# Performance work log

Hardware: AMD Instinct MI355X
Metric: run time of the kernel (lower is better)

## Reference

```python
import jax, jax.numpy as jnp
import numpy as np

N_HEAD = 16

def setup_inputs() -> dict:
    key = jax.random.key(0)
    ks = jax.random.split(key, 7)
    B, T, C = 2, 2048, 1024
    return {
        "query": jax.random.normal(ks[0], (B, T, C), jnp.float32),
        "key": jax.random.normal(ks[1], (B, T, C), jnp.float32),
        "value": jax.random.normal(ks[2], (B, T, C), jnp.float32),
        "Wq": jax.random.normal(ks[3], (C, C), jnp.float32) * (1.0 / np.sqrt(C)),
        "Wk": jax.random.normal(ks[4], (C, C), jnp.float32) * (1.0 / np.sqrt(C)),
        "Wv": jax.random.normal(ks[5], (C, C), jnp.float32) * (1.0 / np.sqrt(C)),
        "Wo": jax.random.normal(ks[6], (C, C), jnp.float32) * (1.0 / np.sqrt(C)),
    }

def reference(query, key, value, Wq, Wk, Wv, Wo):
    B, T, C = query.shape
    H = N_HEAD
    D = C // H
    # QKV projections (torch Linear: x @ W.T, no bias)
    q = (query @ Wq.T).reshape(B, T, H, D).transpose(0, 2, 1, 3)  # [B,H,T,D]
    k = (key   @ Wk.T).reshape(B, T, H, D).transpose(0, 2, 1, 3)
    v = (value @ Wv.T).reshape(B, T, H, D).transpose(0, 2, 1, 3)
    scale = 1.0 / np.sqrt(D).astype(np.float32)
    att = jnp.einsum("bhqd,bhkd->bhqk", q, k) * scale  # [B,H,T,T]
    att = jax.nn.softmax(att, axis=-1)
    y = jnp.einsum("bhqk,bhkd->bhqd", att, v)  # [B,H,T,D]
    y = y.transpose(0, 2, 1, 3).reshape(B, T, C)
    return y @ Wo.T
```

## Files before the change

kernel.cpp:

```cpp
#include <hip/hip_runtime.h>
#include <hip/hip_bf16.h>
#include <cstdint>

typedef __attribute__((ext_vector_type(8))) short bf16x8;
typedef __attribute__((ext_vector_type(4))) float f32x4;
typedef __attribute__((ext_vector_type(16))) float f32x16;
typedef __attribute__((ext_vector_type(4))) unsigned short us4;

#define MFMA16(a, b, c) __builtin_amdgcn_mfma_f32_16x16x32_bf16((a), (b), (c), 0, 0, 0)
#define MFMA32(a, b, c) __builtin_amdgcn_mfma_f32_32x32x16_bf16((a), (b), (c), 0, 0, 0)
#define GLB_PTR(p) ((const __attribute__((address_space(1))) void*)(p))
#define LDS_PTR(p) ((__attribute__((address_space(3))) void*)(p))
#define WAITV(n) asm volatile("s_waitcnt vmcnt(" #n ")" ::: "memory")

__device__ __forceinline__ unsigned short f2bf(float f) {
    union { float f; unsigned u; } v; v.f = f;
    unsigned r = v.u + 0x7fffu + ((v.u >> 16) & 1u);
    return (unsigned short)(r >> 16);
}

__device__ __forceinline__ unsigned cvtpk(float lo, float hi) {
    unsigned r;
    asm("v_cvt_pk_bf16_f32 %0, %1, %2" : "=v"(r) : "v"(lo), "v"(hi));
    return r;
}

struct CastArgs {
    const float* src[7];
    unsigned short* dst[7];
    int n4[7];
};

__global__ __launch_bounds__(256) void cast_f32_bf16(CastArgs a) {
    const int id = blockIdx.y;
    const float4* s = (const float4*)a.src[id];
    us4* d = (us4*)a.dst[id];
    const int n4 = a.n4[id];
    for (int i = blockIdx.x * blockDim.x + threadIdx.x; i < n4;
         i += gridDim.x * blockDim.x) {
        float4 v = s[i];
        us4 o;
        o.x = f2bf(v.x); o.y = f2bf(v.y); o.z = f2bf(v.z); o.w = f2bf(v.w);
        d[i] = o;
    }
}

struct GemmGroup {
    const unsigned short* A[3];
    const unsigned short* B[3];
    unsigned short* C[3];
};

__global__ __launch_bounds__(256, 2)
void gemm_qkv(GemmGroup gg, int M, int N, int K) {
    __shared__ __align__(16) unsigned short As[3][128 * 32];
    __shared__ __align__(16) unsigned short Bs[3][128 * 32];
    const int z = blockIdx.z;
    const unsigned short* __restrict__ A = gg.A[z];
    const unsigned short* __restrict__ B = gg.B[z];
    unsigned short* __restrict__ C = gg.C[z];
    const int t = threadIdx.x;
    const int lane = t & 63, wave = t >> 6;
    const int row0 = blockIdx.x * 128, col0 = blockIdx.y * 128;
    const int wr = (wave >> 1) * 64, wc = (wave & 1) * 64;
    const int r = lane & 15, g = lane >> 4;
    const int srow = t >> 2;
    const int scol = (t & 3) * 8;

#define GSTAGE(sl, k0)                                                         \
    {                                                                          \
        _Pragma("unroll")                                                      \
        for (int i = 0; i < 2; ++i) {                                          \
            const int rr = i * 64 + srow;                                      \
            __builtin_amdgcn_global_load_lds(                                  \
                GLB_PTR(A + (size_t)(row0 + rr) * K + (k0) + scol),            \
                LDS_PTR(&As[sl][rr * 32 + scol]), 16, 0, 0);                   \
            __builtin_amdgcn_global_load_lds(                                  \
                GLB_PTR(B + (size_t)(col0 + rr) * K + (k0) + scol),            \
                LDS_PTR(&Bs[sl][rr * 32 + scol]), 16, 0, 0);                   \
        }                                                                      \
    }

    f32x4 acc[4][4] = {};
    GSTAGE(0, 0);
    GSTAGE(1, 32);

    for (int it = 0; it < 32; ++it) {
        if (it < 31) WAITV(4); else WAITV(0);
        __builtin_amdgcn_s_barrier();
        __builtin_amdgcn_sched_barrier(0);
        if (it + 2 < 32) GSTAGE((it + 2) % 3, (it + 2) * 32);
        const int sl = it % 3;
        bf16x8 a[4], b[4];
#pragma unroll
        for (int m = 0; m < 4; ++m)
            a[m] = *(const bf16x8*)(&As[sl][(wr + m * 16 + r) * 32 + g * 8]);
#pragma unroll
        for (int n = 0; n < 4; ++n)
            b[n] = *(const bf16x8*)(&Bs[sl][(wc + n * 16 + r) * 32 + g * 8]);
        __builtin_amdgcn_s_setprio(1);
#pragma unroll
        for (int m = 0; m < 4; ++m)
#pragma unroll
            for (int n = 0; n < 4; ++n)
                acc[m][n] = MFMA16(a[m], b[n], acc[m][n]);
        __builtin_amdgcn_s_setprio(0);
    }
#undef GSTAGE

    const float sc = (z == 0) ? 0.18033688011112042f : 1.0f;
#pragma unroll
    for (int m = 0; m < 4; ++m) {
#pragma unroll
        for (int n = 0; n < 4; ++n) {
#pragma unroll
            for (int i = 0; i < 4; ++i) {
                const int row = row0 + wr + m * 16 + g * 4 + i;
                const int col = col0 + wc + n * 16 + r;
                const int b_ = row >> 11, tt = row & 2047;
                const int h = col >> 6, d = col & 63;
                const int bh = b_ * 16 + h;
                size_t idx;
                if (z == 2) {
                    const int l = (d & 31) + 32 * ((tt >> 3) & 1);
                    idx = ((((size_t)(bh * 32 + (tt >> 6))) * 2 + (d >> 5)) * 4 +
                           ((tt >> 4) & 3)) * 512 + l * 8 + (tt & 7);
                } else {
                    const int l = (tt & 31) + 32 * ((d >> 3) & 1);
                    idx = (((size_t)(bh * 64 + (tt >> 5))) * 4 + (d >> 4)) * 512 +
                          l * 8 + (d & 7);
                }
                C[idx] = f2bf(acc[m][n][i] * sc);
            }
        }
    }
}

__global__ __launch_bounds__(256, 2)
void gemm_wo(const unsigned short* __restrict__ A,
             const unsigned short* __restrict__ B,
             float* __restrict__ C, int M, int N, int K) {
    __shared__ __align__(16) unsigned short As[3][64 * 32];
    __shared__ __align__(16) unsigned short Bs[3][128 * 32];
    const int t = threadIdx.x;
    const int lane = t & 63, wave = t >> 6;
    const int row0 = blockIdx.x * 64, col0 = blockIdx.y * 128;
    const int wc = wave * 32;
    const int r = lane & 15, g = lane >> 4;
    const int srow = t >> 2;
    const int scol = (t & 3) * 8;

#define WSTAGE(sl, k0)                                                         \
    {                                                                          \
        __builtin_amdgcn_global_load_lds(                                      \
            GLB_PTR(A + (size_t)(row0 + srow) * K + (k0) + scol),              \
            LDS_PTR(&As[sl][srow * 32 + scol]), 16, 0, 0);                     \
        _Pragma("unroll")                                                      \
        for (int i = 0; i < 2; ++i) {                                          \
            const int rr = i * 64 + srow;                                      \
            __builtin_amdgcn_global_load_lds(                                  \
                GLB_PTR(B + (size_t)(col0 + rr) * K + (k0) + scol),            \
                LDS_PTR(&Bs[sl][rr * 32 + scol]), 16, 0, 0);                   \
        }                                                                      \
    }

    f32x4 acc[4][2] = {};
    WSTAGE(0, 0);
    WSTAGE(1, 32);

    for (int it = 0; it < 32; ++it) {
        if (it < 31) WAITV(3); else WAITV(0);
        __builtin_amdgcn_s_barrier();
        __builtin_amdgcn_sched_barrier(0);
        if (it + 2 < 32) WSTAGE((it + 2) % 3, (it + 2) * 32);
        const int sl = it % 3;
        bf16x8 a[4], b[2];
#pragma unroll
        for (int m = 0; m < 4; ++m)
            a[m] = *(const bf16x8*)(&As[sl][(m * 16 + r) * 32 + g * 8]);
#pragma unroll
        for (int n = 0; n < 2; ++n)
            b[n] = *(const bf16x8*)(&Bs[sl][(wc + n * 16 + r) * 32 + g * 8]);
        __builtin_amdgcn_s_setprio(1);
#pragma unroll
        for (int m = 0; m < 4; ++m)
#pragma unroll
            for (int n = 0; n < 2; ++n)
                acc[m][n] = MFMA16(a[m], b[n], acc[m][n]);
        __builtin_amdgcn_s_setprio(0);
    }
#undef WSTAGE

#pragma unroll
    for (int m = 0; m < 4; ++m)
#pragma unroll
        for (int n = 0; n < 2; ++n)
#pragma unroll
            for (int i = 0; i < 4; ++i) {
                const int row = row0 + m * 16 + g * 4 + i;
                const int col = col0 + wc + n * 16 + r;
                C[(size_t)row * N + col] = acc[m][n][i];
            }
}

__global__ __launch_bounds__(256, 2)
void attn_fwd(const unsigned short* __restrict__ Qpk,
              const unsigned short* __restrict__ Kpk,
              const unsigned short* __restrict__ Vpk,
              unsigned short* __restrict__ Y) {
    __shared__ __align__(16) unsigned short kv_lds[4][16][512];
    const int t = threadIdx.x, lane = t & 63, w = t >> 6;
    const int q31 = lane & 31, hi = lane >> 5;

    const int flat = blockIdx.x;
    const int swz = (flat & 7) * 64 + (flat >> 3);
    const int qt = swz & 15, bh = swz >> 4;
    const int qb0 = qt * 128;

    const unsigned short* Qb = Qpk + ((size_t)(bh * 64 + qt * 4 + w)) * 2048;
    const unsigned short* Kb = Kpk + (size_t)bh * 131072;
    const unsigned short* Vb = Vpk + (size_t)bh * 131072;

    bf16x8 qf[4];
#pragma unroll
    for (int s = 0; s < 4; ++s)
        qf[s] = *(const bf16x8*)(Qb + s * 512 + lane * 8);
    WAITV(0);

    f32x16 o0 = {}, o1 = {};
    float l_ = 0.f;

#define STAGE(sl, kv0)                                                         \
    {                                                                          \
        _Pragma("unroll")                                                      \
        for (int i = 0; i < 4; ++i) {                                          \
            const int f = w * 4 + i;                                           \
            const unsigned short* src =                                        \
                (f < 8 ? Kb : Vb) + (kv0) * 64 + (f & 7) * 512 + lane * 8;     \
            __builtin_amdgcn_global_load_lds(                                  \
                GLB_PTR(src), LDS_PTR(&kv_lds[sl][f][lane * 8]), 16, 0, 0);    \
        }                                                                      \
    }

    STAGE(0, 0);
    STAGE(1, 64);
    STAGE(2, 128);

    WAITV(8);
    __builtin_amdgcn_s_barrier();
    __builtin_amdgcn_sched_barrier(0);
    f32x16 sA0, sA1;
    {
        bf16x8 kf[8];
#pragma unroll
        for (int i = 0; i < 8; ++i)
            kf[i] = *(const bf16x8*)(&kv_lds[0][i][lane * 8]);
#pragma unroll
        for (int r = 0; r < 16; ++r) { sA0[r] = -12.f; sA1[r] = -12.f; }
        __builtin_amdgcn_s_setprio(1);
#pragma unroll
        for (int s = 0; s < 4; ++s) sA0 = MFMA32(kf[s], qf[s], sA0);
#pragma unroll
        for (int s = 0; s < 4; ++s) sA1 = MFMA32(kf[4 + s], qf[s], sA1);
        __builtin_amdgcn_s_setprio(0);
    }

    for (int it = 0; it < 32; ++it) {
        if (it < 30) WAITV(4); else WAITV(0);
        __builtin_amdgcn_s_barrier();
        __builtin_amdgcn_sched_barrier(0);
        if (it + 3 < 32) STAGE((it + 3) & 3, (it + 3) * 64);

        f32x16 sN0, sN1;
        if (it + 1 < 32) {
            const int sln = (it + 1) & 3;
            bf16x8 kf[8];
#pragma unroll
            for (int i = 0; i < 8; ++i)
                kf[i] = *(const bf16x8*)(&kv_lds[sln][i][lane * 8]);
#pragma unroll
            for (int r = 0; r < 16; ++r) { sN0[r] = -12.f; sN1[r] = -12.f; }
#pragma unroll
            for (int s = 0; s < 4; ++s) sN0 = MFMA32(kf[s], qf[s], sN0);
#pragma unroll
            for (int s = 0; s < 4; ++s) sN1 = MFMA32(kf[4 + s], qf[s], sN1);
        }

        float p[32];
#pragma unroll
        for (int r = 0; r < 16; ++r) p[r] = __builtin_amdgcn_exp2f(sA0[r]);
#pragma unroll
        for (int r = 0; r < 16; ++r) p[16 + r] = __builtin_amdgcn_exp2f(sA1[r]);

        float sm[16];
#pragma unroll
        for (int r = 0; r < 16; ++r) sm[r] = p[r] + p[16 + r];
#pragma unroll
        for (int d = 8; d > 0; d >>= 1)
#pragma unroll
            for (int r = 0; r < d; ++r) sm[r] += sm[r + d];
        l_ += sm[0] + __shfl_xor(sm[0], 32);

        unsigned c[16];
#pragma unroll
        for (int i = 0; i < 16; ++i) c[i] = cvtpk(p[2 * i], p[2 * i + 1]);

        const int sl = it & 3;
        bf16x8 vf[8];
#pragma unroll
        for (int i = 0; i < 8; ++i)
            vf[i] = *(const bf16x8*)(&kv_lds[sl][8 + i][lane * 8]);

        __builtin_amdgcn_s_setprio(1);
#pragma unroll
        for (int s = 0; s < 4; ++s) {
            const int base = (s >> 1) * 8 + (s & 1) * 4;
            unsigned a0 = c[base + 0], b0 = c[base + 2];
            unsigned a1 = c[base + 1], b1 = c[base + 3];
            asm volatile("v_permlane32_swap_b32 %0, %1" : "+v"(a0), "+v"(b0));
            asm volatile("v_permlane32_swap_b32 %0, %1" : "+v"(a1), "+v"(b1));
            union { unsigned u[4]; bf16x8 v; } pb;
            pb.u[0] = a0; pb.u[1] = a1; pb.u[2] = b0; pb.u[3] = b1;
            o0 = MFMA32(vf[s], pb.v, o0);
            o1 = MFMA32(vf[4 + s], pb.v, o1);
        }
        __builtin_amdgcn_s_setprio(0);

        sA0 = sN0;
        sA1 = sN1;
    }
#undef STAGE

    __syncthreads();

    unsigned short (*yb)[68] = (unsigned short (*)[68])kv_lds;
    const float rinv = 1.0f / l_;
#pragma unroll
    for (int r = 0; r < 16; ++r) {
        const int dd = (r & 3) + 8 * (r >> 2) + 4 * hi;
        yb[w * 32 + q31][dd] = f2bf(o0[r] * rinv);
        yb[w * 32 + q31][32 + dd] = f2bf(o1[r] * rinv);
    }
    __syncthreads();
    const int b_ = bh >> 4, h = bh & 15;
#pragma unroll
    for (int i = 0; i < 8; ++i) {
        const int row = i * 16 + (t >> 4);
        const int col = (t & 15) * 4;
        *(us4*)(Y + ((size_t)(b_ * 2048 + qb0 + row)) * 1024 + h * 64 + col) =
            *(const us4*)(&yb[row][col]);
    }
}

extern "C" void kernel_launch(void* const* d_in, const int* in_sizes, int n_in,
                              void* d_out, int out_size, void* d_ws, size_t ws_size,
                              hipStream_t stream) {
    uint8_t* ws = (uint8_t*)d_ws;
    unsigned short* xq = (unsigned short*)(ws + 0);
    unsigned short* xk = (unsigned short*)(ws + 8388608);
    unsigned short* xv = (unsigned short*)(ws + 16777216);
    unsigned short* wq = (unsigned short*)(ws + 25165824);
    unsigned short* wk = (unsigned short*)(ws + 27262976);
    unsigned short* wv = (unsigned short*)(ws + 29360128);
    unsigned short* wo = (unsigned short*)(ws + 31457280);
    unsigned short* Qp = (unsigned short*)(ws + 33554432);
    unsigned short* Kp = (unsigned short*)(ws + 41943040);
    unsigned short* Vp = (unsigned short*)(ws + 50331648);
    unsigned short* y  = xq;

    CastArgs ca;
    ca.src[0] = (const float*)d_in[0]; ca.dst[0] = xq; ca.n4[0] = 4194304 / 4;
    ca.src[1] = (const float*)d_in[1]; ca.dst[1] = xk; ca.n4[1] = 4194304 / 4;
    ca.src[2] = (const float*)d_in[2]; ca.dst[2] = xv; ca.n4[2] = 4194304 / 4;
    ca.src[3] = (const float*)d_in[3]; ca.dst[3] = wq; ca.n4[3] = 1048576 / 4;
    ca.src[4] = (const float*)d_in[4]; ca.dst[4] = wk; ca.n4[4] = 1048576 / 4;
    ca.src[5] = (const float*)d_in[5]; ca.dst[5] = wv; ca.n4[5] = 1048576 / 4;
    ca.src[6] = (const float*)d_in[6]; ca.dst[6] = wo; ca.n4[6] = 1048576 / 4;
    cast_f32_bf16<<<dim3(512, 7), 256, 0, stream>>>(ca);

    GemmGroup gg;
    gg.A[0] = xq; gg.B[0] = wq; gg.C[0] = Qp;
    gg.A[1] = xk; gg.B[1] = wk; gg.C[1] = Kp;
    gg.A[2] = xv; gg.B[2] = wv; gg.C[2] = Vp;
    gemm_qkv<<<dim3(32, 8, 3), 256, 0, stream>>>(gg, 4096, 1024, 1024);

    attn_fwd<<<dim3(512), 256, 0, stream>>>(Qp, Kp, Vp, y);

    gemm_wo<<<dim3(64, 8), 256, 0, stream>>>(y, wo, (float*)d_out, 4096, 1024, 1024);
}
```

Measured before the change: 123.1 us.

## Fuse activation fp32-to-bf16 cast into QKV GEMM via fp32 LDS staging

Activations are no longer cast to bf16 in a separate pass. The QKV GEMM now loads fp32 activation tiles straight into LDS with an XOR-swizzled layout and converts them to bf16 in registers with v_cvt_pk before the MFMA. Only the weights are still cast in a smaller kernel. This removes a full read and write of the three activation tensors, at the cost of double the global and LDS traffic per A tile, extra conversion instructions in the inner loop, and a larger LDS footprint that may lower occupancy.

```diff
diff --git a/kernel.cpp b/kernel.cpp
--- a/kernel.cpp
+++ b/kernel.cpp
@@ -26,17 +26,15 @@
 }
 
 struct CastArgs {
-    const float* src[7];
-    unsigned short* dst[7];
-    int n4[7];
+    const float* src[4];
+    unsigned short* dst[4];
 };
 
-__global__ __launch_bounds__(256) void cast_f32_bf16(CastArgs a) {
+__global__ __launch_bounds__(256) void cast_w(CastArgs a) {
     const int id = blockIdx.y;
     const float4* s = (const float4*)a.src[id];
     us4* d = (us4*)a.dst[id];
-    const int n4 = a.n4[id];
-    for (int i = blockIdx.x * blockDim.x + threadIdx.x; i < n4;
+    for (int i = blockIdx.x * blockDim.x + threadIdx.x; i < 262144;
          i += gridDim.x * blockDim.x) {
         float4 v = s[i];
         us4 o;
@@ -46,17 +44,17 @@
 }
 
 struct GemmGroup {
-    const unsigned short* A[3];
+    const float* A[3];
     const unsigned short* B[3];
     unsigned short* C[3];
 };
 
 __global__ __launch_bounds__(256, 2)
-void gemm_qkv(GemmGroup gg, int M, int N, int K) {
-    __shared__ __align__(16) unsigned short As[3][128 * 32];
+void gemm_qkv(GemmGroup gg) {
+    __shared__ __align__(16) float Afs[3][128 * 32];
     __shared__ __align__(16) unsigned short Bs[3][128 * 32];
     const int z = blockIdx.z;
-    const unsigned short* __restrict__ A = gg.A[z];
+    const float* __restrict__ A = gg.A[z];
     const unsigned short* __restrict__ B = gg.B[z];
     unsigned short* __restrict__ C = gg.C[z];
     const int t = threadIdx.x;
@@ -66,17 +64,22 @@
     const int r = lane & 15, g = lane >> 4;
     const int srow = t >> 2;
     const int scol = (t & 3) * 8;
+    const int csrc = (lane & 7) ^ (lane >> 3);
 
 #define GSTAGE(sl, k0)                                                         \
     {                                                                          \
+        _Pragma("unroll")                                                      \
+        for (int j = 0; j < 4; ++j) {                                          \
+            const int rl = wave * 32 + j * 8 + (lane >> 3);                    \
+            __builtin_amdgcn_global_load_lds(                                  \
+                GLB_PTR(A + (size_t)(row0 + rl) * 1024 + (k0) + csrc * 4),     \
+                LDS_PTR(&Afs[sl][rl * 32 + (lane & 7) * 4]), 16, 0, 0);        \
+        }                                                                      \
         _Pragma("unroll")                                                      \
         for (int i = 0; i < 2; ++i) {                                          \
             const int rr = i * 64 + srow;                                      \
             __builtin_amdgcn_global_load_lds(                                  \
-                GLB_PTR(A + (size_t)(row0 + rr) * K + (k0) + scol),            \
-                LDS_PTR(&As[sl][rr * 32 + scol]), 16, 0, 0);                   \
-            __builtin_amdgcn_global_load_lds(                                  \
-                GLB_PTR(B + (size_t)(col0 + rr) * K + (k0) + scol),            \
+                GLB_PTR(B + (size_t)(col0 + rr) * 1024 + (k0) + scol),         \
                 LDS_PTR(&Bs[sl][rr * 32 + scol]), 16, 0, 0);                   \
         }                                                                      \
     }
@@ -86,15 +89,25 @@
     GSTAGE(1, 32);
 
     for (int it = 0; it < 32; ++it) {
-        if (it < 31) WAITV(4); else WAITV(0);
+        if (it < 31) WAITV(6); else WAITV(0);
         __builtin_amdgcn_s_barrier();
         __builtin_amdgcn_sched_barrier(0);
         if (it + 2 < 32) GSTAGE((it + 2) % 3, (it + 2) * 32);
         const int sl = it % 3;
         bf16x8 a[4], b[4];
 #pragma unroll
-        for (int m = 0; m < 4; ++m)
-            a[m] = *(const bf16x8*)(&As[sl][(wr + m * 16 + r) * 32 + g * 8]);
+        for (int m = 0; m < 4; ++m) {
+            const int lr = wr + m * 16 + r;
+            const int x = r & 7;
+            const float4 va = *(const float4*)(&Afs[sl][lr * 32 + ((2 * g) ^ x) * 4]);
+            const float4 vb = *(const float4*)(&Afs[sl][lr * 32 + ((2 * g + 1) ^ x) * 4]);
+            union { unsigned u[4]; bf16x8 v; } cv;
+            cv.u[0] = cvtpk(va.x, va.y);
+            cv.u[1] = cvtpk(va.z, va.w);
+            cv.u[2] = cvtpk(vb.x, vb.y);
+            cv.u[3] = cvtpk(vb.z, vb.w);
+            a[m] = cv.v;
+        }
 #pragma unroll
         for (int n = 0; n < 4; ++n)
             b[n] = *(const bf16x8*)(&Bs[sl][(wc + n * 16 + r) * 32 + g * 8]);
@@ -356,33 +369,27 @@
                               void* d_out, int out_size, void* d_ws, size_t ws_size,
                               hipStream_t stream) {
     uint8_t* ws = (uint8_t*)d_ws;
-    unsigned short* xq = (unsigned short*)(ws + 0);
-    unsigned short* xk = (unsigned short*)(ws + 8388608);
-    unsigned short* xv = (unsigned short*)(ws + 16777216);
-    unsigned short* wq = (unsigned short*)(ws + 25165824);
-    unsigned short* wk = (unsigned short*)(ws + 27262976);
-    unsigned short* wv = (unsigned short*)(ws + 29360128);
-    unsigned short* wo = (unsigned short*)(ws + 31457280);
-    unsigned short* Qp = (unsigned short*)(ws + 33554432);
-    unsigned short* Kp = (unsigned short*)(ws + 41943040);
-    unsigned short* Vp = (unsigned short*)(ws + 50331648);
-    unsigned short* y  = xq;
+    unsigned short* y  = (unsigned short*)(ws + 0);
+    unsigned short* wq = (unsigned short*)(ws + 8388608);
+    unsigned short* wk = (unsigned short*)(ws + 10485760);
+    unsigned short* wv = (unsigned short*)(ws + 12582912);
+    unsigned short* wo = (unsigned short*)(ws + 14680064);
+    unsigned short* Qp = (unsigned short*)(ws + 16777216);
+    unsigned short* Kp = (unsigned short*)(ws + 25165824);
+    unsigned short* Vp = (unsigned short*)(ws + 33554432);
 
     CastArgs ca;
-    ca.src[0] = (const float*)d_in[0]; ca.dst[0] = xq; ca.n4[0] = 4194304 / 4;
-    ca.src[1] = (const float*)d_in[1]; ca.dst[1] = xk; ca.n4[1] = 4194304 / 4;
-    ca.src[2] = (const float*)d_in[2]; ca.dst[2] = xv; ca.n4[2] = 4194304 / 4;
-    ca.src[3] = (const float*)d_in[3]; ca.dst[3] = wq; ca.n4[3] = 1048576 / 4;
-    ca.src[4] = (const float*)d_in[4]; ca.dst[4] = wk; ca.n4[4] = 1048576 / 4;
-    ca.src[5] = (const float*)d_in[5]; ca.dst[5] = wv; ca.n4[5] = 1048576 / 4;
-    ca.src[6] = (const float*)d_in[6]; ca.dst[6] = wo; ca.n4[6] = 1048576 / 4;
-    cast_f32_bf16<<<dim3(512, 7), 256, 0, stream>>>(ca);
+    ca.src[0] = (const float*)d_in[3]; ca.dst[0] = wq;
+    ca.src[1] = (const float*)d_in[4]; ca.dst[1] = wk;
+    ca.src[2] = (const float*)d_in[5]; ca.dst[2] = wv;
+    ca.src[3] = (const float*)d_in[6]; ca.dst[3] = wo;
+    cast_w<<<dim3(64, 4), 256, 0, stream>>>(ca);
 
     GemmGroup gg;
-    gg.A[0] = xq; gg.B[0] = wq; gg.C[0] = Qp;
-    gg.A[1] = xk; gg.B[1] = wk; gg.C[1] = Kp;
-    gg.A[2] = xv; gg.B[2] = wv; gg.C[2] = Vp;
-    gemm_qkv<<<dim3(32, 8, 3), 256, 0, stream>>>(gg, 4096, 1024, 1024);
+    gg.A[0] = (const float*)d_in[0]; gg.B[0] = wq; gg.C[0] = Qp;
+    gg.A[1] = (const float*)d_in[1]; gg.B[1] = wk; gg.C[1] = Kp;
+    gg.A[2] = (const float*)d_in[2]; gg.B[2] = wv; gg.C[2] = Vp;
+    gemm_qkv<<<dim3(32, 8, 3), 256, 0, stream>>>(gg);
 
     attn_fwd<<<dim3(512), 256, 0, stream>>>(Qp, Kp, Vp, y);
 
```

Result: slower. 140.1 us (+13.8%).
